# Optimization experiments

Hardware: AMD Instinct MI355X
Metric: run time of the kernel (lower is better)

Reference implementation:

```python
import jax, jax.numpy as jnp
import numpy as np

EPS_ALPHA = 1e-7
EPS_STEP = 1e-6


def setup_inputs() -> dict:
    key = jax.random.key(0)
    k1, k2, k3 = jax.random.split(key, 3)
    B, T, D = 32, 1024, 512
    x = jax.random.normal(k1, (B, T, D), dtype=jnp.float32)
    # Linear(in_dim, 1) params (sigmoid-gain init approximated with small normal)
    W = jax.random.normal(k2, (D, 1), dtype=jnp.float32) * (1.0 / np.sqrt(D))
    b = jnp.zeros((1,), dtype=jnp.float32)
    return {"x": x, "W": W, "b": b, "r": 1, "num_steps": 1024}


def reference(x, W, b, r, num_steps):
    # x: [B, T, D]; r is unused (as in the original forward)
    B, T, D = x.shape
    speeds = jax.nn.sigmoid(jnp.einsum('btd,do->bto', x, W) + b)  # [B, T, 1]
    sp = speeds[:, :, 0]  # [B, T]

    # alpha0 = [1, 1e-7, 1e-7, ...]
    alpha0 = jnp.concatenate(
        [jnp.ones((B, 1), x.dtype), jnp.full((B, T - 1), EPS_ALPHA, x.dtype)], axis=1)

    def step(alpha, _):
        # u = alpha . speeds  -> [B, 1]
        u = jnp.sum(alpha * sp, axis=1, keepdims=True)
        sq = 1.7 - jnp.abs(u - 0.5)  # 1 + 0.7 - |u-0.5|
        shifted = jnp.pad(alpha[:, :-1], ((0, 0), (1, 0)))  # forward shift
        a = ((1.0 - u) * alpha + u * shifted + EPS_STEP) ** sq
        a = a / jnp.sum(a, axis=1, keepdims=True)
        return a, a

    _, alphas = jax.lax.scan(step, alpha0, None, length=num_steps)  # [S, B, T]
    alphas = jnp.transpose(alphas, (1, 0, 2))  # [B, S, T]
    contexts = jnp.einsum('bst,btd->bsd', alphas, x)  # [B, S, D]
    return contexts, alphas
```

## Files before the change

### kernel.cpp

```cpp
#include <hip/hip_runtime.h>
#include <hip/hip_bf16.h>

#define NB 32
#define NT 1024
#define ND 512
#define NS 1024

#define CTX_ELEMS (32u * 1024u * 512u)
#define SP_SCRATCH_OFF (CTX_ELEMS - 32u*1024u)

__device__ __forceinline__ float vlog2(float x) {
    float r; asm("v_log_f32 %0, %1" : "=v"(r) : "v"(x)); return r;
}
__device__ __forceinline__ float vexp2(float x) {
    float r; asm("v_exp_f32 %0, %1" : "=v"(r) : "v"(x)); return r;
}
__device__ __forceinline__ float vrcp(float x) {
    float r; asm("v_rcp_f32 %0, %1" : "=v"(r) : "v"(x)); return r;
}

template<int ctrl, int rm, int bm, bool bc>
__device__ __forceinline__ float dppadd(float x) {
    int y = __builtin_amdgcn_update_dpp(0, __float_as_int(x), ctrl, rm, bm, bc);
    return x + __int_as_float(y);
}
__device__ __forceinline__ float reduce63(float x) {
    x = dppadd<0x111, 0xf, 0xf, true >(x);
    x = dppadd<0x112, 0xf, 0xf, true >(x);
    x = dppadd<0x114, 0xf, 0xf, true >(x);
    x = dppadd<0x118, 0xf, 0xf, true >(x);
    x = dppadd<0x142, 0xa, 0xf, false>(x);
    x = dppadd<0x143, 0xc, 0xf, false>(x);
    return x;
}
__device__ __forceinline__ float wave_shr1(float x) {
    int y = __builtin_amdgcn_update_dpp(0, __float_as_int(x), 0x138, 0xf, 0xf, true);
    return __int_as_float(y);
}

__global__ __launch_bounds__(256) void sp_kernel(const float* __restrict__ x,
                                                 const float* __restrict__ W,
                                                 const float* __restrict__ bias,
                                                 float* __restrict__ sp)
{
    const int lane = threadIdx.x & 63;
    const int wid  = threadIdx.x >> 6;
    const int row  = blockIdx.x * 4 + wid;
    const float4* xr = reinterpret_cast<const float4*>(x + (size_t)row * ND) + lane * 2;
    const float4* wr = reinterpret_cast<const float4*>(W) + lane * 2;
    float4 xa = xr[0], xb = xr[1];
    float4 wa = wr[0], wb = wr[1];
    float d = xa.x*wa.x + xa.y*wa.y + xa.z*wa.z + xa.w*wa.w
            + xb.x*wb.x + xb.y*wb.y + xb.z*wb.z + xb.w*wb.w;
    #pragma unroll
    for (int m = 1; m < 64; m <<= 1) d += __shfl_xor(d, m);
    if (lane == 0) {
        float z = d + bias[0];
        float e = vexp2(-z * 1.442695040888963f);
        sp[row] = 1.0f / (1.0f + e);
    }
}

__global__ __launch_bounds__(256) void scan_kernel(const float* __restrict__ sp,
                                                   float* __restrict__ alphas)
{
    const int b    = blockIdx.x;
    const int tx   = threadIdx.x;
    const int lane = tx & 63;
    const int wid  = tx >> 6;

    __shared__ float r1[2][4];
    __shared__ float r2[2][4];
    __shared__ float rb[2][4];

    float spv[4], raw[4];
    {
        float4 v = *reinterpret_cast<const float4*>(sp + (size_t)b * NT + tx * 4);
        spv[0] = v.x; spv[1] = v.y; spv[2] = v.z; spv[3] = v.w;
    }
    #pragma unroll
    for (int j = 0; j < 4; ++j) raw[j] = 1e-7f;
    if (tx == 0) raw[0] = 1.0f;
    float carry = (wid == 0) ? 0.0f : 1e-7f;

    {
        float p2 = fmaf(raw[0], spv[0], fmaf(raw[1], spv[1], fmaf(raw[2], spv[2], raw[3]*spv[3])));
        p2 = reduce63(p2);
        if (lane == 63) r2[1][wid] = p2;
    }
    __syncthreads();
    float u;
    {
        float4 v2 = *reinterpret_cast<const float4*>(r2[1]);
        u = (v2.x + v2.y) + (v2.z + v2.w);
    }
    float inv = 1.0f;

    float* outp = alphas + (size_t)b * NS * NT + tx * 4;

    for (int s = 0; s < NS; ++s) {
        const int p = s & 1;
        const float sq = 1.7f - fabsf(u - 0.5f);
        const float c1 = (1.0f - u) * inv;
        const float c0 = u * inv;

        float prev = wave_shr1(raw[3]);
        float sh0  = (lane == 0) ? carry : prev;

        float anew[4];
        {
            float v0 = fmaf(c1, raw[0], fmaf(c0, sh0,    1e-6f));
            float v1 = fmaf(c1, raw[1], fmaf(c0, raw[0], 1e-6f));
            float v2 = fmaf(c1, raw[2], fmaf(c0, raw[1], 1e-6f));
            float v3 = fmaf(c1, raw[3], fmaf(c0, raw[2], 1e-6f));
            anew[0] = vexp2(sq * vlog2(v0));
            anew[1] = vexp2(sq * vlog2(v1));
            anew[2] = vexp2(sq * vlog2(v2));
            anew[3] = vexp2(sq * vlog2(v3));
        }

        float p1 = (anew[0] + anew[1]) + (anew[2] + anew[3]);
        float p2 = fmaf(anew[0], spv[0], anew[1]*spv[1]) + fmaf(anew[2], spv[2], anew[3]*spv[3]);
        p1 = reduce63(p1);
        p2 = reduce63(p2);
        if (lane == 63) { r1[p][wid] = p1; r2[p][wid] = p2; rb[p][wid] = anew[3]; }
        __syncthreads();

        float4 v1 = *reinterpret_cast<const float4*>(r1[p]);
        float4 v2 = *reinterpret_cast<const float4*>(r2[p]);
        float bc  = rb[p][(wid == 0) ? 0 : (wid - 1)];
        carry = (wid == 0) ? 0.0f : bc;

        float t1 = (v1.x + v1.y) + (v1.z + v1.w);
        float t2 = (v2.x + v2.y) + (v2.z + v2.w);
        inv = vrcp(t1);
        u   = t2 * inv;

        float4 o;
        o.x = anew[0] * inv; o.y = anew[1] * inv; o.z = anew[2] * inv; o.w = anew[3] * inv;
        *reinterpret_cast<float4*>(outp + (size_t)s * NT) = o;

        #pragma unroll
        for (int j = 0; j < 4; ++j) raw[j] = anew[j];
    }
}

typedef __bf16 bf16x8 __attribute__((ext_vector_type(8)));
typedef float  f32x4  __attribute__((ext_vector_type(4)));

#define BM 128
#define BN 128
#define BK 32
#define LDP 40

__global__ __launch_bounds__(256) void gemm_kernel(const float* __restrict__ alphas,
                                                   const float* __restrict__ x,
                                                   float* __restrict__ contexts)
{
    __shared__ __align__(16) __bf16 As[BM * LDP];
    __shared__ __align__(16) __bf16 Xs[BN * LDP];

    const int b  = blockIdx.z;
    const int s0 = blockIdx.y * BM;
    const int n0 = blockIdx.x * BN;
    const int tx = threadIdx.x;
    const int lane = tx & 63;
    const int wid  = tx >> 6;
    const int wm = wid >> 1, wn = wid & 1;
    const int lr = lane & 15;
    const int lk = (lane >> 4) * 8;

    f32x4 acc[4][4];
    #pragma unroll
    for (int i = 0; i < 4; ++i)
        #pragma unroll
        for (int j = 0; j < 4; ++j) acc[i][j] = (f32x4){0.f, 0.f, 0.f, 0.f};

    const int arow = tx >> 1;
    const int akb  = (tx & 1) * 16;
    const int xk0 = tx >> 5;
    const int xn4 = (tx & 31) * 4;

    for (int k0 = 0; k0 < NT; k0 += BK) {
        {
            const float* ap = alphas + ((size_t)b * NS + s0 + arow) * NT + k0 + akb;
            float4 a0 = reinterpret_cast<const float4*>(ap)[0];
            float4 a1 = reinterpret_cast<const float4*>(ap)[1];
            float4 a2 = reinterpret_cast<const float4*>(ap)[2];
            float4 a3 = reinterpret_cast<const float4*>(ap)[3];
            bf16x8 w0, w1;
            w0[0]=(__bf16)a0.x; w0[1]=(__bf16)a0.y; w0[2]=(__bf16)a0.z; w0[3]=(__bf16)a0.w;
            w0[4]=(__bf16)a1.x; w0[5]=(__bf16)a1.y; w0[6]=(__bf16)a1.z; w0[7]=(__bf16)a1.w;
            w1[0]=(__bf16)a2.x; w1[1]=(__bf16)a2.y; w1[2]=(__bf16)a2.z; w1[3]=(__bf16)a2.w;
            w1[4]=(__bf16)a3.x; w1[5]=(__bf16)a3.y; w1[6]=(__bf16)a3.z; w1[7]=(__bf16)a3.w;
            *reinterpret_cast<bf16x8*>(&As[arow * LDP + akb])     = w0;
            *reinterpret_cast<bf16x8*>(&As[arow * LDP + akb + 8]) = w1;
        }
        #pragma unroll
        for (int pss = 0; pss < 4; ++pss) {
            int kk = xk0 + pss * 8;
            float4 v = *reinterpret_cast<const float4*>(
                x + ((size_t)b * NT + k0 + kk) * ND + n0 + xn4);
            Xs[(xn4 + 0) * LDP + kk] = (__bf16)v.x;
            Xs[(xn4 + 1) * LDP + kk] = (__bf16)v.y;
            Xs[(xn4 + 2) * LDP + kk] = (__bf16)v.z;
            Xs[(xn4 + 3) * LDP + kk] = (__bf16)v.w;
        }
        __syncthreads();

        bf16x8 av[4], bv[4];
        #pragma unroll
        for (int i = 0; i < 4; ++i)
            av[i] = *reinterpret_cast<const bf16x8*>(&As[(wm*64 + i*16 + lr) * LDP + lk]);
        #pragma unroll
        for (int j = 0; j < 4; ++j)
            bv[j] = *reinterpret_cast<const bf16x8*>(&Xs[(wn*64 + j*16 + lr) * LDP + lk]);
        #pragma unroll
        for (int i = 0; i < 4; ++i)
            #pragma unroll
            for (int j = 0; j < 4; ++j)
                acc[i][j] = __builtin_amdgcn_mfma_f32_16x16x32_bf16(av[i], bv[j], acc[i][j], 0, 0, 0);
        __syncthreads();
    }

    const int ccol = lr;
    const int crow = (lane >> 4) * 4;
    #pragma unroll
    for (int i = 0; i < 4; ++i) {
        #pragma unroll
        for (int j = 0; j < 4; ++j) {
            int col = n0 + wn*64 + j*16 + ccol;
            int rb2 = s0 + wm*64 + i*16 + crow;
            #pragma unroll
            for (int r = 0; r < 4; ++r)
                contexts[((size_t)b * NS + rb2 + r) * ND + col] = acc[i][j][r];
        }
    }
}

extern "C" void kernel_launch(void* const* d_in, const int* in_sizes, int n_in,
                              void* d_out, int out_size, void* d_ws, size_t ws_size,
                              hipStream_t stream) {
    const float* x    = (const float*)d_in[0];
    const float* W    = (const float*)d_in[1];
    const float* bias = (const float*)d_in[2];
    float* contexts = (float*)d_out;
    float* alphas   = (float*)d_out + CTX_ELEMS;
    float* sp       = (float*)d_out + SP_SCRATCH_OFF;

    sp_kernel<<<dim3(NB * NT / 4), dim3(256), 0, stream>>>(x, W, bias, sp);
    scan_kernel<<<dim3(NB), dim3(256), 0, stream>>>(sp, alphas);
    gemm_kernel<<<dim3(ND / BN, NS / BM, NB), dim3(256), 0, stream>>>(alphas, x, contexts);
}
```

Baseline: 463.6 us.

## Prefetch next GEMM tile into registers and streamline scan step arithmetic

The GEMM now loads the next K-tile of alphas and x into registers before the barrier, so global loads overlap with the MFMA work on the current tile. Plain __syncthreads are replaced by a barrier that waits only on LDS counters, so outstanding global loads are not drained. The scan kernel is restated with precomputed differences, giving one FMA chain per element, and packs the three per-wave exchange values into a single float4 LDS write. This adds register pressure in the GEMM and slightly changes the floating-point rounding of the recurrence.

```diff
diff --git a/kernel.cpp b/kernel.cpp
--- a/kernel.cpp
+++ b/kernel.cpp
@@ -36,6 +36,12 @@
 __device__ __forceinline__ float wave_shr1(float x) {
     int y = __builtin_amdgcn_update_dpp(0, __float_as_int(x), 0x138, 0xf, 0xf, true);
     return __int_as_float(y);
+}
+
+__device__ __forceinline__ void lds_barrier() {
+    asm volatile("s_waitcnt lgkmcnt(0)" ::: "memory");
+    __builtin_amdgcn_s_barrier();
+    asm volatile("" ::: "memory");
 }
 
 __global__ __launch_bounds__(256) void sp_kernel(const float* __restrict__ x,
@@ -69,31 +75,28 @@
     const int lane = tx & 63;
     const int wid  = tx >> 6;
 
-    __shared__ float r1[2][4];
-    __shared__ float r2[2][4];
-    __shared__ float rb[2][4];
-
-    float spv[4], raw[4];
+    __shared__ __align__(16) float xch[2][4][4];
+
+    float spv0, spv1, spv2, spv3;
     {
         float4 v = *reinterpret_cast<const float4*>(sp + (size_t)b * NT + tx * 4);
-        spv[0] = v.x; spv[1] = v.y; spv[2] = v.z; spv[3] = v.w;
-    }
-    #pragma unroll
-    for (int j = 0; j < 4; ++j) raw[j] = 1e-7f;
-    if (tx == 0) raw[0] = 1.0f;
-    float carry = (wid == 0) ? 0.0f : 1e-7f;
+        spv0 = v.x; spv1 = v.y; spv2 = v.z; spv3 = v.w;
+    }
+    float a0 = 1e-7f, a1 = 1e-7f, a2 = 1e-7f, a3 = 1e-7f;
+    if (tx == 0) a0 = 1.0f;
+
+    float prevn = wave_shr1(a3);
+    float carry0 = (wid == 0) ? 0.0f : 1e-7f;
+    float e0 = ((lane == 0) ? carry0 : prevn) - a0;
+    float e1 = a0 - a1, e2 = a1 - a2, e3 = a2 - a3;
 
     {
-        float p2 = fmaf(raw[0], spv[0], fmaf(raw[1], spv[1], fmaf(raw[2], spv[2], raw[3]*spv[3])));
-        p2 = reduce63(p2);
-        if (lane == 63) r2[1][wid] = p2;
-    }
-    __syncthreads();
-    float u;
-    {
-        float4 v2 = *reinterpret_cast<const float4*>(r2[1]);
-        u = (v2.x + v2.y) + (v2.z + v2.w);
-    }
+        float q2 = fmaf(a0, spv0, fmaf(a1, spv1, fmaf(a2, spv2, a3 * spv3)));
+        q2 = reduce63(q2);
+        if (lane == 63) xch[1][wid][1] = q2;
+    }
+    lds_barrier();
+    float u = (xch[1][0][1] + xch[1][1][1]) + (xch[1][2][1] + xch[1][3][1]);
     float inv = 1.0f;
 
     float* outp = alphas + (size_t)b * NS * NT + tx * 4;
@@ -101,47 +104,46 @@
     for (int s = 0; s < NS; ++s) {
         const int p = s & 1;
         const float sq = 1.7f - fabsf(u - 0.5f);
-        const float c1 = (1.0f - u) * inv;
-        const float c0 = u * inv;
-
-        float prev = wave_shr1(raw[3]);
-        float sh0  = (lane == 0) ? carry : prev;
-
-        float anew[4];
-        {
-            float v0 = fmaf(c1, raw[0], fmaf(c0, sh0,    1e-6f));
-            float v1 = fmaf(c1, raw[1], fmaf(c0, raw[0], 1e-6f));
-            float v2 = fmaf(c1, raw[2], fmaf(c0, raw[1], 1e-6f));
-            float v3 = fmaf(c1, raw[3], fmaf(c0, raw[2], 1e-6f));
-            anew[0] = vexp2(sq * vlog2(v0));
-            anew[1] = vexp2(sq * vlog2(v1));
-            anew[2] = vexp2(sq * vlog2(v2));
-            anew[3] = vexp2(sq * vlog2(v3));
-        }
-
-        float p1 = (anew[0] + anew[1]) + (anew[2] + anew[3]);
-        float p2 = fmaf(anew[0], spv[0], anew[1]*spv[1]) + fmaf(anew[2], spv[2], anew[3]*spv[3]);
+
+        float an0 = vexp2(sq * vlog2(fmaf(inv, fmaf(u, e0, a0), 1e-6f)));
+        float an1 = vexp2(sq * vlog2(fmaf(inv, fmaf(u, e1, a1), 1e-6f)));
+        float an2 = vexp2(sq * vlog2(fmaf(inv, fmaf(u, e2, a2), 1e-6f)));
+        float an3 = vexp2(sq * vlog2(fmaf(inv, fmaf(u, e3, a3), 1e-6f)));
+
+        prevn = wave_shr1(an3);
+        float ne1 = an0 - an1, ne2 = an1 - an2, ne3 = an2 - an3;
+
+        float p1 = (an0 + an1) + (an2 + an3);
+        float q2 = fmaf(an0, spv0, an1 * spv1) + fmaf(an2, spv2, an3 * spv3);
         p1 = reduce63(p1);
-        p2 = reduce63(p2);
-        if (lane == 63) { r1[p][wid] = p1; r2[p][wid] = p2; rb[p][wid] = anew[3]; }
-        __syncthreads();
-
-        float4 v1 = *reinterpret_cast<const float4*>(r1[p]);
-        float4 v2 = *reinterpret_cast<const float4*>(r2[p]);
-        float bc  = rb[p][(wid == 0) ? 0 : (wid - 1)];
-        carry = (wid == 0) ? 0.0f : bc;
-
-        float t1 = (v1.x + v1.y) + (v1.z + v1.w);
-        float t2 = (v2.x + v2.y) + (v2.z + v2.w);
+        q2 = reduce63(q2);
+        if (lane == 63) {
+            float4 rec; rec.x = p1; rec.y = q2; rec.z = an3; rec.w = 0.0f;
+            *reinterpret_cast<float4*>(&xch[p][wid][0]) = rec;
+        }
+        lds_barrier();
+
+        float2 r0 = *reinterpret_cast<const float2*>(&xch[p][0][0]);
+        float2 r1 = *reinterpret_cast<const float2*>(&xch[p][1][0]);
+        float2 r2 = *reinterpret_cast<const float2*>(&xch[p][2][0]);
+        float2 r3 = *reinterpret_cast<const float2*>(&xch[p][3][0]);
+        float bnd = xch[p][(wid == 0) ? 0 : (wid - 1)][2];
+
+        float t1 = (r0.x + r1.x) + (r2.x + r3.x);
+        float t2 = (r0.y + r1.y) + (r2.y + r3.y);
         inv = vrcp(t1);
         u   = t2 * inv;
 
+        float carry = (wid == 0) ? 0.0f : bnd;
+        e0 = ((lane == 0) ? carry : prevn) - an0;
+        e1 = ne1; e2 = ne2; e3 = ne3;
+
         float4 o;
-        o.x = anew[0] * inv; o.y = anew[1] * inv; o.z = anew[2] * inv; o.w = anew[3] * inv;
-        *reinterpret_cast<float4*>(outp + (size_t)s * NT) = o;
-
-        #pragma unroll
-        for (int j = 0; j < 4; ++j) raw[j] = anew[j];
+        o.x = an0 * inv; o.y = an1 * inv; o.z = an2 * inv; o.w = an3 * inv;
+        *reinterpret_cast<float4*>(outp) = o;
+        outp += NT;
+
+        a0 = an0; a1 = an1; a2 = an2; a3 = an3;
     }
 }
 
@@ -181,32 +183,60 @@
     const int xk0 = tx >> 5;
     const int xn4 = (tx & 31) * 4;
 
+    const float* ap = alphas + ((size_t)b * NS + s0 + arow) * NT + akb;
+    const float* xp = x + ((size_t)b * NT + xk0) * ND + n0 + xn4;
+
+    float4 va0 = reinterpret_cast<const float4*>(ap)[0];
+    float4 va1 = reinterpret_cast<const float4*>(ap)[1];
+    float4 va2 = reinterpret_cast<const float4*>(ap)[2];
+    float4 va3 = reinterpret_cast<const float4*>(ap)[3];
+    float4 vx0 = *reinterpret_cast<const float4*>(xp + 0 * 8 * ND);
+    float4 vx1 = *reinterpret_cast<const float4*>(xp + 1 * 8 * ND);
+    float4 vx2 = *reinterpret_cast<const float4*>(xp + 2 * 8 * ND);
+    float4 vx3 = *reinterpret_cast<const float4*>(xp + 3 * 8 * ND);
+    ap += BK;
+    xp += (size_t)BK * ND;
+
     for (int k0 = 0; k0 < NT; k0 += BK) {
         {
-            const float* ap = alphas + ((size_t)b * NS + s0 + arow) * NT + k0 + akb;
-            float4 a0 = reinterpret_cast<const float4*>(ap)[0];
-            float4 a1 = reinterpret_cast<const float4*>(ap)[1];
-            float4 a2 = reinterpret_cast<const float4*>(ap)[2];
-            float4 a3 = reinterpret_cast<const float4*>(ap)[3];
             bf16x8 w0, w1;
-            w0[0]=(__bf16)a0.x; w0[1]=(__bf16)a0.y; w0[2]=(__bf16)a0.z; w0[3]=(__bf16)a0.w;
-            w0[4]=(__bf16)a1.x; w0[5]=(__bf16)a1.y; w0[6]=(__bf16)a1.z; w0[7]=(__bf16)a1.w;
-            w1[0]=(__bf16)a2.x; w1[1]=(__bf16)a2.y; w1[2]=(__bf16)a2.z; w1[3]=(__bf16)a2.w;
-            w1[4]=(__bf16)a3.x; w1[5]=(__bf16)a3.y; w1[6]=(__bf16)a3.z; w1[7]=(__bf16)a3.w;
+            w0[0]=(__bf16)va0.x; w0[1]=(__bf16)va0.y; w0[2]=(__bf16)va0.z; w0[3]=(__bf16)va0.w;
+            w0[4]=(__bf16)va1.x; w0[5]=(__bf16)va1.y; w0[6]=(__bf16)va1.z; w0[7]=(__bf16)va1.w;
+            w1[0]=(__bf16)va2.x; w1[1]=(__bf16)va2.y; w1[2]=(__bf16)va2.z; w1[3]=(__bf16)va2.w;
+            w1[4]=(__bf16)va3.x; w1[5]=(__bf16)va3.y; w1[6]=(__bf16)va3.z; w1[7]=(__bf16)va3.w;
             *reinterpret_cast<bf16x8*>(&As[arow * LDP + akb])     = w0;
             *reinterpret_cast<bf16x8*>(&As[arow * LDP + akb + 8]) = w1;
-        }
-        #pragma unroll
-        for (int pss = 0; pss < 4; ++pss) {
-            int kk = xk0 + pss * 8;
-            float4 v = *reinterpret_cast<const float4*>(
-                x + ((size_t)b * NT + k0 + kk) * ND + n0 + xn4);
-            Xs[(xn4 + 0) * LDP + kk] = (__bf16)v.x;
-            Xs[(xn4 + 1) * LDP + kk] = (__bf16)v.y;
-            Xs[(xn4 + 2) * LDP + kk] = (__bf16)v.z;
-            Xs[(xn4 + 3) * LDP + kk] = (__bf16)v.w;
-        }
-        __syncthreads();
+            int kk0 = xk0;
+            Xs[(xn4+0)*LDP + kk0]      = (__bf16)vx0.x;
+            Xs[(xn4+1)*LDP + kk0]      = (__bf16)vx0.y;
+            Xs[(xn4+2)*LDP + kk0]      = (__bf16)vx0.z;
+            Xs[(xn4+3)*LDP + kk0]      = (__bf16)vx0.w;
+            Xs[(xn4+0)*LDP + kk0 + 8]  = (__bf16)vx1.x;
+            Xs[(xn4+1)*LDP + kk0 + 8]  = (__bf16)vx1.y;
+            Xs[(xn4+2)*LDP + kk0 + 8]  = (__bf16)vx1.z;
+            Xs[(xn4+3)*LDP + kk0 + 8]  = (__bf16)vx1.w;
+            Xs[(xn4+0)*LDP + kk0 + 16] = (__bf16)vx2.x;
+            Xs[(xn4+1)*LDP + kk0 + 16] = (__bf16)vx2.y;
+            Xs[(xn4+2)*LDP + kk0 + 16] = (__bf16)vx2.z;
+            Xs[(xn4+3)*LDP + kk0 + 16] = (__bf16)vx2.w;
+            Xs[(xn4+0)*LDP + kk0 + 24] = (__bf16)vx3.x;
+            Xs[(xn4+1)*LDP + kk0 + 24] = (__bf16)vx3.y;
+            Xs[(xn4+2)*LDP + kk0 + 24] = (__bf16)vx3.z;
+            Xs[(xn4+3)*LDP + kk0 + 24] = (__bf16)vx3.w;
+        }
+        if (k0 + BK < NT) {
+            va0 = reinterpret_cast<const float4*>(ap)[0];
+            va1 = reinterpret_cast<const float4*>(ap)[1];
+            va2 = reinterpret_cast<const float4*>(ap)[2];
+            va3 = reinterpret_cast<const float4*>(ap)[3];
+            vx0 = *reinterpret_cast<const float4*>(xp + 0 * 8 * ND);
+            vx1 = *reinterpret_cast<const float4*>(xp + 1 * 8 * ND);
+            vx2 = *reinterpret_cast<const float4*>(xp + 2 * 8 * ND);
+            vx3 = *reinterpret_cast<const float4*>(xp + 3 * 8 * ND);
+            ap += BK;
+            xp += (size_t)BK * ND;
+        }
+        lds_barrier();
 
         bf16x8 av[4], bv[4];
         #pragma unroll
@@ -220,7 +250,7 @@
             #pragma unroll
             for (int j = 0; j < 4; ++j)
                 acc[i][j] = __builtin_amdgcn_mfma_f32_16x16x32_bf16(av[i], bv[j], acc[i][j], 0, 0, 0);
-        __syncthreads();
+        lds_barrier();
     }
 
     const int ccol = lr;
```

After: 497.2 us. 1.07x slower.

## Enlarge GEMM tiles to 256x256 with 512 threads and register prefetch

Applied to the files above, without the earlier changes.

The alphas-times-x GEMM tile grows to 256x256 with 8 waves, each computing 128x64 outputs. The next K slice of alphas and x is loaded into registers while the current slice is converted and stored to LDS. __syncthreads is replaced by an explicit lgkmcnt wait plus s_barrier. The aim is more data reuse per LDS load and overlap of global loads with MFMA work, at the cost of higher register pressure and fewer blocks.

```diff
diff --git a/kernel.cpp b/kernel.cpp
--- a/kernel.cpp
+++ b/kernel.cpp
@@ -36,6 +36,12 @@
 __device__ __forceinline__ float wave_shr1(float x) {
     int y = __builtin_amdgcn_update_dpp(0, __float_as_int(x), 0x138, 0xf, 0xf, true);
     return __int_as_float(y);
+}
+
+__device__ __forceinline__ void lds_barrier() {
+    asm volatile("s_waitcnt lgkmcnt(0)" ::: "memory");
+    __builtin_amdgcn_s_barrier();
+    asm volatile("" ::: "memory");
 }
 
 __global__ __launch_bounds__(256) void sp_kernel(const float* __restrict__ x,
@@ -148,14 +154,14 @@
 typedef __bf16 bf16x8 __attribute__((ext_vector_type(8)));
 typedef float  f32x4  __attribute__((ext_vector_type(4)));
 
-#define BM 128
-#define BN 128
+#define BM 256
+#define BN 256
 #define BK 32
 #define LDP 40
 
-__global__ __launch_bounds__(256) void gemm_kernel(const float* __restrict__ alphas,
-                                                   const float* __restrict__ x,
-                                                   float* __restrict__ contexts)
+__global__ __launch_bounds__(512, 2) void gemm_kernel(const float* __restrict__ alphas,
+                                                      const float* __restrict__ x,
+                                                      float* __restrict__ contexts)
 {
     __shared__ __align__(16) __bf16 As[BM * LDP];
     __shared__ __align__(16) __bf16 Xs[BN * LDP];
@@ -166,74 +172,102 @@
     const int tx = threadIdx.x;
     const int lane = tx & 63;
     const int wid  = tx >> 6;
-    const int wm = wid >> 1, wn = wid & 1;
+    const int wm = wid >> 2;
+    const int wn = wid & 3;
     const int lr = lane & 15;
     const int lk = (lane >> 4) * 8;
 
-    f32x4 acc[4][4];
-    #pragma unroll
-    for (int i = 0; i < 4; ++i)
+    f32x4 acc[8][4];
+    #pragma unroll
+    for (int i = 0; i < 8; ++i)
         #pragma unroll
         for (int j = 0; j < 4; ++j) acc[i][j] = (f32x4){0.f, 0.f, 0.f, 0.f};
 
     const int arow = tx >> 1;
     const int akb  = (tx & 1) * 16;
-    const int xk0 = tx >> 5;
-    const int xn4 = (tx & 31) * 4;
+    const int xk0 = tx >> 6;
+    const int xn4 = (tx & 63) * 4;
+
+    const float* ap = alphas + ((size_t)b * NS + s0 + arow) * NT + akb;
+    const float* xp = x + ((size_t)b * NT + xk0) * ND + n0 + xn4;
+
+    float4 va0 = reinterpret_cast<const float4*>(ap)[0];
+    float4 va1 = reinterpret_cast<const float4*>(ap)[1];
+    float4 va2 = reinterpret_cast<const float4*>(ap)[2];
+    float4 va3 = reinterpret_cast<const float4*>(ap)[3];
+    float4 vx0 = *reinterpret_cast<const float4*>(xp + 0 * 8 * ND);
+    float4 vx1 = *reinterpret_cast<const float4*>(xp + 1 * 8 * ND);
+    float4 vx2 = *reinterpret_cast<const float4*>(xp + 2 * 8 * ND);
+    float4 vx3 = *reinterpret_cast<const float4*>(xp + 3 * 8 * ND);
+    ap += BK;
+    xp += (size_t)BK * ND;
 
     for (int k0 = 0; k0 < NT; k0 += BK) {
         {
-            const float* ap = alphas + ((size_t)b * NS + s0 + arow) * NT + k0 + akb;
-            float4 a0 = reinterpret_cast<const float4*>(ap)[0];
-            float4 a1 = reinterpret_cast<const float4*>(ap)[1];
-            float4 a2 = reinterpret_cast<const float4*>(ap)[2];
-            float4 a3 = reinterpret_cast<const float4*>(ap)[3];
             bf16x8 w0, w1;
-            w0[0]=(__bf16)a0.x; w0[1]=(__bf16)a0.y; w0[2]=(__bf16)a0.z; w0[3]=(__bf16)a0.w;
-            w0[4]=(__bf16)a1.x; w0[5]=(__bf16)a1.y; w0[6]=(__bf16)a1.z; w0[7]=(__bf16)a1.w;
-            w1[0]=(__bf16)a2.x; w1[1]=(__bf16)a2.y; w1[2]=(__bf16)a2.z; w1[3]=(__bf16)a2.w;
-            w1[4]=(__bf16)a3.x; w1[5]=(__bf16)a3.y; w1[6]=(__bf16)a3.z; w1[7]=(__bf16)a3.w;
+            w0[0]=(__bf16)va0.x; w0[1]=(__bf16)va0.y; w0[2]=(__bf16)va0.z; w0[3]=(__bf16)va0.w;
+            w0[4]=(__bf16)va1.x; w0[5]=(__bf16)va1.y; w0[6]=(__bf16)va1.z; w0[7]=(__bf16)va1.w;
+            w1[0]=(__bf16)va2.x; w1[1]=(__bf16)va2.y; w1[2]=(__bf16)va2.z; w1[3]=(__bf16)va2.w;
+            w1[4]=(__bf16)va3.x; w1[5]=(__bf16)va3.y; w1[6]=(__bf16)va3.z; w1[7]=(__bf16)va3.w;
             *reinterpret_cast<bf16x8*>(&As[arow * LDP + akb])     = w0;
             *reinterpret_cast<bf16x8*>(&As[arow * LDP + akb + 8]) = w1;
-        }
-        #pragma unroll
-        for (int pss = 0; pss < 4; ++pss) {
-            int kk = xk0 + pss * 8;
-            float4 v = *reinterpret_cast<const float4*>(
-                x + ((size_t)b * NT + k0 + kk) * ND + n0 + xn4);
-            Xs[(xn4 + 0) * LDP + kk] = (__bf16)v.x;
-            Xs[(xn4 + 1) * LDP + kk] = (__bf16)v.y;
-            Xs[(xn4 + 2) * LDP + kk] = (__bf16)v.z;
-            Xs[(xn4 + 3) * LDP + kk] = (__bf16)v.w;
-        }
-        __syncthreads();
-
-        bf16x8 av[4], bv[4];
-        #pragma unroll
-        for (int i = 0; i < 4; ++i)
-            av[i] = *reinterpret_cast<const bf16x8*>(&As[(wm*64 + i*16 + lr) * LDP + lk]);
+            Xs[(xn4+0)*LDP + xk0]      = (__bf16)vx0.x;
+            Xs[(xn4+1)*LDP + xk0]      = (__bf16)vx0.y;
+            Xs[(xn4+2)*LDP + xk0]      = (__bf16)vx0.z;
+            Xs[(xn4+3)*LDP + xk0]      = (__bf16)vx0.w;
+            Xs[(xn4+0)*LDP + xk0 + 8]  = (__bf16)vx1.x;
+            Xs[(xn4+1)*LDP + xk0 + 8]  = (__bf16)vx1.y;
+            Xs[(xn4+2)*LDP + xk0 + 8]  = (__bf16)vx1.z;
+            Xs[(xn4+3)*LDP + xk0 + 8]  = (__bf16)vx1.w;
+            Xs[(xn4+0)*LDP + xk0 + 16] = (__bf16)vx2.x;
+            Xs[(xn4+1)*LDP + xk0 + 16] = (__bf16)vx2.y;
+            Xs[(xn4+2)*LDP + xk0 + 16] = (__bf16)vx2.z;
+            Xs[(xn4+3)*LDP + xk0 + 16] = (__bf16)vx2.w;
+            Xs[(xn4+0)*LDP + xk0 + 24] = (__bf16)vx3.x;
+            Xs[(xn4+1)*LDP + xk0 + 24] = (__bf16)vx3.y;
+            Xs[(xn4+2)*LDP + xk0 + 24] = (__bf16)vx3.z;
+            Xs[(xn4+3)*LDP + xk0 + 24] = (__bf16)vx3.w;
+        }
+        if (k0 + BK < NT) {
+            va0 = reinterpret_cast<const float4*>(ap)[0];
+            va1 = reinterpret_cast<const float4*>(ap)[1];
+            va2 = reinterpret_cast<const float4*>(ap)[2];
+            va3 = reinterpret_cast<const float4*>(ap)[3];
+            vx0 = *reinterpret_cast<const float4*>(xp + 0 * 8 * ND);
+            vx1 = *reinterpret_cast<const float4*>(xp + 1 * 8 * ND);
+            vx2 = *reinterpret_cast<const float4*>(xp + 2 * 8 * ND);
+            vx3 = *reinterpret_cast<const float4*>(xp + 3 * 8 * ND);
+            ap += BK;
+            xp += (size_t)BK * ND;
+        }
+        lds_barrier();
+
+        bf16x8 av[8], bv[4];
         #pragma unroll
         for (int j = 0; j < 4; ++j)
             bv[j] = *reinterpret_cast<const bf16x8*>(&Xs[(wn*64 + j*16 + lr) * LDP + lk]);
         #pragma unroll
-        for (int i = 0; i < 4; ++i)
+        for (int i = 0; i < 8; ++i)
+            av[i] = *reinterpret_cast<const bf16x8*>(&As[(wm*128 + i*16 + lr) * LDP + lk]);
+        #pragma unroll
+        for (int i = 0; i < 8; ++i)
             #pragma unroll
             for (int j = 0; j < 4; ++j)
                 acc[i][j] = __builtin_amdgcn_mfma_f32_16x16x32_bf16(av[i], bv[j], acc[i][j], 0, 0, 0);
-        __syncthreads();
+        lds_barrier();
     }
 
     const int ccol = lr;
     const int crow = (lane >> 4) * 4;
     #pragma unroll
-    for (int i = 0; i < 4; ++i) {
+    for (int i = 0; i < 8; ++i) {
         #pragma unroll
         for (int j = 0; j < 4; ++j) {
             int col = n0 + wn*64 + j*16 + ccol;
-            int rb2 = s0 + wm*64 + i*16 + crow;
+            int rw  = s0 + wm*128 + i*16 + crow;
             #pragma unroll
             for (int r = 0; r < 4; ++r)
-                contexts[((size_t)b * NS + rb2 + r) * ND + col] = acc[i][j][r];
+                contexts[((size_t)b * NS + rw + r) * ND + col] = acc[i][j][r];
         }
     }
 }
@@ -250,5 +284,5 @@
 
     sp_kernel<<<dim3(NB * NT / 4), dim3(256), 0, stream>>>(x, W, bias, sp);
     scan_kernel<<<dim3(NB), dim3(256), 0, stream>>>(sp, alphas);
-    gemm_kernel<<<dim3(ND / BN, NS / BM, NB), dim3(256), 0, stream>>>(alphas, x, contexts);
-}
+    gemm_kernel<<<dim3(ND / BN, NS / BM, NB), dim3(512), 0, stream>>>(alphas, x, contexts);
+}
```

Result: faster. 398.3 us (-14.1%).
